# Kernel optimization log

Hardware: AMD Instinct MI355X
Metric: run time of the kernel (lower is better)

The kernel has to match this reference:

```python
import jax, jax.numpy as jnp
import numpy as np
from jax import lax

DEPTH = 5
LEAF = 2 ** DEPTH          # 32
GATES = LEAF - 1           # 31
LATENT = 128
IN_SHAPE = (128, 8, 8)     # C, H, W after mixture reshape
OUT_FEAT = IN_SHAPE[0] * IN_SHAPE[1] * IN_SHAPE[2]  # 8192
BATCH = 512


def conv_t(x, w, b):
    # PyTorch ConvTranspose2d(k=4, s=2, p=1): weight layout [in, out, kh, kw].
    # Equivalent fwd conv: flip spatial dims, swap in/out, lhs_dilation=2, pad k-1-p=2.
    w_ = jnp.flip(w, (2, 3)).transpose(1, 0, 2, 3)  # [out, in, kh, kw]
    y = lax.conv_general_dilated(
        x, w_, window_strides=(1, 1), padding=((2, 2), (2, 2)),
        lhs_dilation=(2, 2), dimension_numbers=("NCHW", "OIHW", "NCHW"))
    return y + b[None, :, None, None]


def leaf_probs_fn(x, gw, gb):
    # gatings: [B, GATES]
    g = jax.nn.sigmoid(x @ gw + gb)
    dens = jnp.ones((x.shape[0], 1), dtype=x.dtype)  # root density
    start = 0
    for d in range(1, DEPTH + 1):
        n_par = 2 ** (d - 1)
        gp = lax.dynamic_slice_in_dim(g, start, n_par, axis=1)  # [B, n_par]
        # left child (odd node index) uses g, right child uses 1-g, interleaved.
        dens = jnp.stack([dens * gp, dens * (1.0 - gp)], axis=-1).reshape(x.shape[0], 2 * n_par)
        start += n_par
    return dens  # [B, LEAF]


def setup_inputs() -> dict:
    key = jax.random.key(0)
    ks = jax.random.split(key, 10)
    C = IN_SHAPE[0]
    inp = {
        "x": jax.random.normal(ks[0], (BATCH, LATENT), dtype=jnp.float32),
        # SoftTree gating params (kaiming-normal ~ N(0, sqrt(2/fan_in)) approx)
        "gw": jax.random.normal(ks[1], (LATENT, GATES), dtype=jnp.float32) * (2.0 / LATENT) ** 0.5,
        "gb": jnp.zeros((GATES,), dtype=jnp.float32),
        # constant projection leaves
        "z": jax.random.normal(ks[2], (OUT_FEAT, LEAF), dtype=jnp.float32),
        # ConvTranspose2d weights, PyTorch layout [in_ch, out_ch, kh, kw]
        "w1": jax.random.normal(ks[3], (C, 128, 4, 4), dtype=jnp.float32) * 0.02,
        "b1": jnp.zeros((128,), dtype=jnp.float32),
        "w2": jax.random.normal(ks[4], (128, 64, 4, 4), dtype=jnp.float32) * 0.02,
        "b2": jnp.zeros((64,), dtype=jnp.float32),
        "w3": jax.random.normal(ks[5], (64, 3, 4, 4), dtype=jnp.float32) * 0.02,
        "b3": jnp.zeros((3,), dtype=jnp.float32),
    }
    return inp


def reference(x, gw, gb, z, w1, b1, w2, b2, w3, b3):
    lp = leaf_probs_fn(x, gw, gb)              # [B, LEAF]
    out = lp @ z.T                              # [B, OUT_FEAT] == (z @ lp.T).T
    out = out.reshape(-1, *IN_SHAPE)            # [B, 128, 8, 8]
    out = jax.nn.relu(conv_t(out, w1, b1))      # [B, 128, 16, 16]
    out = jax.nn.relu(conv_t(out, w2, b2))      # [B, 64, 32, 32]
    out = conv_t(out, w3, b3)                   # [B, 3, 64, 64]
    return out
```

## Files before the change

### kernel.cpp

```cpp
#include <hip/hip_runtime.h>
#include <hip/hip_bf16.h>
#include <stdint.h>

using bf16 = __hip_bfloat16;
typedef __attribute__((ext_vector_type(8))) short bf16x8;
typedef __attribute__((ext_vector_type(4))) float f32x4;
typedef __attribute__((ext_vector_type(16))) float f32x16;

#define BATCHN 512

__device__ __forceinline__ void zero_halo_dev(bf16* buf, int H, int W, int C, int idx) {
  int nvec = C >> 3;
  int P = 2 * (W + 2) + 2 * H;
  if (idx >= BATCHN * P * nvec) return;
  int cv = idx % nvec;
  int p = (idx / nvec) % P;
  int b = idx / (nvec * P);
  int row, col;
  if (p < W + 2) { row = 0; col = p; }
  else if (p < 2 * (W + 2)) { row = H + 1; col = p - (W + 2); }
  else { int q = p - 2 * (W + 2); row = 1 + (q >> 1); col = (q & 1) ? (W + 1) : 0; }
  float4 z4 = {0.f, 0.f, 0.f, 0.f};
  *(float4*)(buf + ((size_t)(b * (H + 2) + row) * (W + 2) + col) * C + cv * 8) = z4;
}

__device__ __forceinline__ void wprep_dev(const float* w, bf16* wt, int IC, int OCr, int OCp, int idx) {
  int KG = IC / 8;
  if (idx >= 16 * OCp * IC) return;
  int e = idx & 7;
  int t = idx >> 3;
  int oc = t % OCp; t /= OCp;
  int kg = t % KG; t /= KG;
  int tap = t & 3, p = t >> 2;
  int ic = kg * 8 + e;
  int dy = tap >> 1, dx = tap & 1;
  int py = p >> 1, px = p & 1;
  const int ktab[2][2] = {{1, 3}, {2, 0}};
  int ky = ktab[py][dy], kx = ktab[px][dx];
  float v = 0.f;
  if (oc < OCr) v = w[((ic * OCr + oc) * 4 + ky) * 4 + kx];
  wt[idx] = __float2bfloat16(v);
}

#define NB_Z1 1152
#define NB_Z2 2176
#define NB_Z3 2112
#define NB_W1 1024
#define NB_W2 512
#define NB_W3 64
#define NB_G  128

__global__ void prep_kernel(bf16* x1, bf16* x2, bf16* x3,
                            const float* w1, bf16* wt1, const float* w2, bf16* wt2,
                            const float* w3, bf16* wt3,
                            const float* x, const float* gw, const float* gb, float* lp) {
  int bid = blockIdx.x;
  int tid = threadIdx.x;
  if (bid < NB_Z1) { zero_halo_dev(x1, 8, 8, 128, bid * 256 + tid); return; }
  bid -= NB_Z1;
  if (bid < NB_Z2) { zero_halo_dev(x2, 16, 16, 128, bid * 256 + tid); return; }
  bid -= NB_Z2;
  if (bid < NB_Z3) { zero_halo_dev(x3, 32, 32, 64, bid * 256 + tid); return; }
  bid -= NB_Z3;
  if (bid < NB_W1) { wprep_dev(w1, wt1, 128, 128, 128, bid * 256 + tid); return; }
  bid -= NB_W1;
  if (bid < NB_W2) { wprep_dev(w2, wt2, 128, 64, 64, bid * 256 + tid); return; }
  bid -= NB_W2;
  if (bid < NB_W3) { wprep_dev(w3, wt3, 64, 3, 16, bid * 256 + tid); return; }
  bid -= NB_W3;
  __shared__ float xs[4][128];
  __shared__ float gs[4][32];
  const int sub = tid >> 6, t = tid & 63;
  const int b = bid * 4 + sub;
  xs[sub][t] = x[b * 128 + t];
  xs[sub][t + 64] = x[b * 128 + 64 + t];
  __syncthreads();
  if (t < 31) {
    float acc = gb[t];
    #pragma unroll 8
    for (int k = 0; k < 128; ++k) acc += xs[sub][k] * gw[k * 31 + t];
    gs[sub][t] = 1.f / (1.f + __expf(-acc));
  }
  __syncthreads();
  if (t < 32) {
    float prob = 1.f;
    #pragma unroll
    for (int d = 1; d <= 5; ++d) {
      int i = t >> (6 - d);
      int node = (1 << (d - 1)) - 1 + i;
      float gv = gs[sub][node];
      prob *= ((t >> (5 - d)) & 1) ? (1.f - gv) : gv;
    }
    lp[b * 32 + t] = prob;
  }
}

__global__ void mixture_kernel(const float* __restrict__ z, const float* __restrict__ lp,
                               bf16* __restrict__ x1) {
  __shared__ float lps[64 * 32];
  const int s = blockIdx.x;
  const int h = s >> 3, w = s & 7;
  const int b0 = blockIdx.y * 64;
  const int t = threadIdx.x;
  const int c = t & 127;
  const int half = t >> 7;
  float4 zr[8];
  const float4* zp = (const float4*)(z + (size_t)(c * 64 + s) * 32);
  #pragma unroll
  for (int i = 0; i < 8; ++i) zr[i] = zp[i];
  #pragma unroll
  for (int i = 0; i < 8; ++i) lps[t + 256 * i] = lp[b0 * 32 + t + 256 * i];
  __syncthreads();
  for (int bs = 0; bs < 32; ++bs) {
    int bl = half * 32 + bs;
    const float4* lr = (const float4*)(lps + bl * 32);
    float acc = 0.f;
    #pragma unroll
    for (int i = 0; i < 8; ++i) {
      float4 l4 = lr[i];
      acc += zr[i].x * l4.x + zr[i].y * l4.y + zr[i].z * l4.z + zr[i].w * l4.w;
    }
    int b = b0 + bl;
    x1[((size_t)(b * 10 + h + 1) * 10 + (w + 1)) * 128 + c] = __float2bfloat16(acc);
  }
}

#define CLASS_TABLES \
  constexpr int TAPA[9] = {0, 1, 1, 2, 2, 3, 3, 3, 3}; \
  constexpr int DYA[9]  = {0, 0, 0,-1, 1,-1,-1, 1, 1}; \
  constexpr int DXA[9]  = {0,-1, 1, 0, 0,-1, 1,-1, 1}; \
  constexpr int MSK[9]  = {0xF,0x5,0xA,0x3,0xC,0x1,0x2,0x4,0x8};

template<int IC, int OCp, int IH, int IW, int ROWS>
__global__ __launch_bounds__(256, 3)
void convt32(const bf16* __restrict__ xin, const bf16* __restrict__ wt,
             const float* __restrict__ bias, bf16* __restrict__ xout) {
  constexpr int KG = IC / 8;
  constexpr int NS = IC / 16;
  constexpr int IH2 = IH + 2, IW2 = IW + 2;
  constexpr int OH2 = 2 * IH + 2, OW2 = 2 * IW + 2;
  constexpr int NPIX = (ROWS + 2) * IW2;
  constexpr int BPI = IH / ROWS;
  constexpr int LIW = (IW == 8 ? 3 : 4);
  constexpr int ICV = IC / 8;
  __shared__ bf16 Alds[KG * NPIX * 8];

  const int tid = threadIdx.x;
  const int wave = tid >> 6, lane = tid & 63;
  const int hl = lane >> 5, l32 = lane & 31;
  const int wm = wave >> 1, wn = wave & 1;
  const int img = blockIdx.x / BPI;
  const int tb = blockIdx.x % BPI;
  const int n0 = blockIdx.y * 64;

  const bf16* src = xin + ((size_t)img * IH2 + tb * ROWS) * IW2 * IC;
  for (int g = tid; g < NPIX * ICV; g += 256) {
    const int pix = g / ICV;
    const int gr = g % ICV;
    const float4 v = *(const float4*)(src + (size_t)g * 8);
    *(float4*)(&Alds[(gr * NPIX + pix) * 8]) = v;
  }

  const int m = wm * 32 + l32;
  const int cpix = ((m >> LIW) + 1) * IW2 + (m & (IW - 1)) + 1;
  const bf16* wtp = wt + (size_t)(n0 + wn * 32 + l32) * 8;

  f32x16 acc[4];
  #pragma unroll
  for (int p = 0; p < 4; ++p)
    #pragma unroll
    for (int r = 0; r < 16; ++r) acc[p][r] = 0.f;

  CLASS_TABLES
  __syncthreads();

  #pragma unroll
  for (int e = 0; e < 9; ++e) {
    const int tap = TAPA[e];
    const int sh = (DYA[e] * IW2 + DXA[e]);
    #pragma unroll
    for (int s = 0; s < NS; ++s) {
      const bf16x8 a = *(const bf16x8*)(Alds + (((s * 2 + hl) * NPIX) + cpix + sh) * 8);
      #pragma unroll
      for (int p = 0; p < 4; ++p) {
        if (MSK[e] & (1 << p)) {
          const int chunk = p * 4 + tap;
          const bf16x8 b = *(const bf16x8*)(wtp + ((size_t)(chunk * KG + s * 2 + hl) * OCp) * 8);
          acc[p] = __builtin_amdgcn_mfma_f32_32x32x16_bf16(a, b, acc[p], 0, 0, 0);
        }
      }
    }
  }

  const int oc = n0 + wn * 32 + l32;
  const float bv = bias[oc];
  #pragma unroll
  for (int p = 0; p < 4; ++p) {
    const int py = p >> 1, px = p & 1;
    #pragma unroll
    for (int r = 0; r < 16; ++r) {
      const int ml = wm * 32 + (r & 3) + 8 * (r >> 2) + 4 * hl;
      const int y = tb * ROWS + (ml >> LIW), x = ml & (IW - 1);
      float v = fmaxf(acc[p][r] + bv, 0.f);
      xout[(((size_t)img * OH2 + 2 * y + py + 1) * OW2 + 2 * x + px + 1) * OCp + oc] =
          __float2bfloat16(v);
    }
  }
}

__global__ __launch_bounds__(256, 3)
void convt16_final(const bf16* __restrict__ xin, const bf16* __restrict__ wt,
                   const float* __restrict__ bias, float* __restrict__ fout) {
  constexpr int IC = 64, OCp = 16, OCr = 3, IH = 32, IW = 32, ROWS = 8;
  constexpr int KG = IC / 8;
  constexpr int NC = IC / 32;
  constexpr int IH2 = IH + 2, IW2 = IW + 2;
  constexpr int NPIX = (ROWS + 2) * IW2;
  constexpr int BPI = IH / ROWS;
  constexpr int MI = 4;
  constexpr int ICV = IC / 8;
  __shared__ bf16 Alds[KG * NPIX * 8];

  const int tid = threadIdx.x;
  const int wave = tid >> 6, lane = tid & 63;
  const int q = lane >> 4, li = lane & 15;
  const int img = blockIdx.x / BPI;
  const int tb = blockIdx.x % BPI;

  const bf16* src = xin + ((size_t)img * IH2 + tb * ROWS) * IW2 * IC;
  for (int g = tid; g < NPIX * ICV; g += 256) {
    const int pix = g / ICV;
    const int gr = g % ICV;
    const float4 v = *(const float4*)(src + (size_t)g * 8);
    *(float4*)(&Alds[(gr * NPIX + pix) * 8]) = v;
  }

  int cpix[MI];
  #pragma unroll
  for (int mi = 0; mi < MI; ++mi) {
    const int m = wave * 64 + mi * 16 + li;
    cpix[mi] = ((m >> 5) + 1) * IW2 + (m & 31) + 1;
  }
  const bf16* wtp = wt + (size_t)li * 8;

  f32x4 acc[4][MI];
  #pragma unroll
  for (int p = 0; p < 4; ++p)
    #pragma unroll
    for (int mi = 0; mi < MI; ++mi)
      acc[p][mi] = (f32x4){0.f, 0.f, 0.f, 0.f};

  CLASS_TABLES
  __syncthreads();

  #pragma unroll
  for (int e = 0; e < 9; ++e) {
    const int tap = TAPA[e];
    const int sh = (DYA[e] * IW2 + DXA[e]);
    #pragma unroll
    for (int c = 0; c < NC; ++c) {
      bf16x8 bfr[4];
      #pragma unroll
      for (int p = 0; p < 4; ++p)
        if (MSK[e] & (1 << p))
          bfr[p] = *(const bf16x8*)(wtp + ((size_t)((p * 4 + tap) * KG + c * 4 + q) * OCp) * 8);
      #pragma unroll
      for (int mi = 0; mi < MI; ++mi) {
        const bf16x8 a = *(const bf16x8*)(Alds + (((c * 4 + q) * NPIX) + cpix[mi] + sh) * 8);
        #pragma unroll
        for (int p = 0; p < 4; ++p)
          if (MSK[e] & (1 << p))
            acc[p][mi] = __builtin_amdgcn_mfma_f32_16x16x32_bf16(a, bfr[p], acc[p][mi], 0, 0, 0);
      }
    }
  }

  const int oc = li;
  if (oc < OCr) {
    const float bv = bias[oc];
    #pragma unroll
    for (int py = 0; py < 2; ++py)
      #pragma unroll
      for (int mi = 0; mi < MI; ++mi)
        #pragma unroll
        for (int r = 0; r < 4; ++r) {
          const int pix = (wave * MI + mi) * 16 + q * 4 + r;
          const int y = tb * ROWS + (pix >> 5), x = pix & 31;
          float2 v2;
          v2.x = acc[py * 2 + 0][mi][r] + bv;
          v2.y = acc[py * 2 + 1][mi][r] + bv;
          *(float2*)(&fout[(((size_t)img * 3 + oc) * 64 + 2 * y + py) * 64 + 2 * x]) = v2;
        }
  }
}

extern "C" void kernel_launch(void* const* d_in, const int* in_sizes, int n_in,
                              void* d_out, int out_size, void* d_ws, size_t ws_size,
                              hipStream_t stream) {
  const float* x  = (const float*)d_in[0];
  const float* gw = (const float*)d_in[1];
  const float* gb = (const float*)d_in[2];
  const float* z  = (const float*)d_in[3];
  const float* w1 = (const float*)d_in[4];
  const float* b1 = (const float*)d_in[5];
  const float* w2 = (const float*)d_in[6];
  const float* b2 = (const float*)d_in[7];
  const float* w3 = (const float*)d_in[8];
  const float* b3 = (const float*)d_in[9];
  float* out = (float*)d_out;

  char* w = (char*)d_ws;
  float* lp  = (float*)(w);
  bf16* x1  = (bf16*)(w + 65536);
  bf16* x2  = (bf16*)(w + 13172736);
  bf16* x3  = (bf16*)(w + 55640064);
  bf16* wt1 = (bf16*)(w + 131399680);
  bf16* wt2 = (bf16*)(w + 131923968);
  bf16* wt3 = (bf16*)(w + 132186112);

  prep_kernel<<<NB_Z1 + NB_Z2 + NB_Z3 + NB_W1 + NB_W2 + NB_W3 + NB_G, 256, 0, stream>>>(
      x1, x2, x3, w1, wt1, w2, wt2, w3, wt3, x, gw, gb, lp);

  mixture_kernel<<<dim3(64, 8), 256, 0, stream>>>(z, lp, x1);

  convt32<128, 128, 8, 8, 8><<<dim3(512, 2), 256, 0, stream>>>(x1, wt1, b1, x2);
  convt32<128, 64, 16, 16, 4><<<dim3(2048, 1), 256, 0, stream>>>(x2, wt2, b2, x3);
  convt16_final<<<dim3(2048, 1), 256, 0, stream>>>(x3, wt3, b3, out);
}
```

Baseline: 218.5 us.

## Restructure conv-transpose kernels so each wave owns one output parity

The first two transposed-conv layers move from a 256-thread kernel, where each wave handled a 32-row M slice across all four output parities, to a 512-thread kernel. In the new kernel each wave owns one parity and a 32-wide OC slice and accumulates several 32-row M tiles (MI). Each weight fragment is now loaded once per k-step and reused across MI MFMAs, and the next B fragment is prefetched while the current one is used. Layer 1 packs two images per block and layer 2 uses taller row tiles. The trade-off is more accumulator registers per thread (MI f32x16 accumulators) and larger LDS tiles, which may reduce occupancy.

```diff
diff --git a/kernel.cpp b/kernel.cpp
--- a/kernel.cpp
+++ b/kernel.cpp
@@ -125,84 +125,93 @@
   }
 }
 
-#define CLASS_TABLES \
-  constexpr int TAPA[9] = {0, 1, 1, 2, 2, 3, 3, 3, 3}; \
-  constexpr int DYA[9]  = {0, 0, 0,-1, 1,-1,-1, 1, 1}; \
-  constexpr int DXA[9]  = {0,-1, 1, 0, 0,-1, 1,-1, 1}; \
-  constexpr int MSK[9]  = {0xF,0x5,0xA,0x3,0xC,0x1,0x2,0x4,0x8};
-
-template<int IC, int OCp, int IH, int IW, int ROWS>
-__global__ __launch_bounds__(256, 3)
-void convt32(const bf16* __restrict__ xin, const bf16* __restrict__ wt,
-             const float* __restrict__ bias, bf16* __restrict__ xout) {
+template<int IC, int OCp, int IH, int IW, int ROWS, int IMGS>
+__global__ __launch_bounds__(512, 4)
+void convt32s(const bf16* __restrict__ xin, const bf16* __restrict__ wt,
+              const float* __restrict__ bias, bf16* __restrict__ xout) {
   constexpr int KG = IC / 8;
   constexpr int NS = IC / 16;
   constexpr int IH2 = IH + 2, IW2 = IW + 2;
   constexpr int OH2 = 2 * IH + 2, OW2 = 2 * IW + 2;
-  constexpr int NPIX = (ROWS + 2) * IW2;
+  constexpr int TPIX = (ROWS + 2) * IW2;
+  constexpr int NPIXT = IMGS * TPIX;
   constexpr int BPI = IH / ROWS;
+  constexpr int MI = IMGS * ROWS * IW / 32;
   constexpr int LIW = (IW == 8 ? 3 : 4);
   constexpr int ICV = IC / 8;
-  __shared__ bf16 Alds[KG * NPIX * 8];
+  __shared__ bf16 Alds[KG * NPIXT * 8];
 
   const int tid = threadIdx.x;
   const int wave = tid >> 6, lane = tid & 63;
-  const int hl = lane >> 5, l32 = lane & 31;
-  const int wm = wave >> 1, wn = wave & 1;
-  const int img = blockIdx.x / BPI;
-  const int tb = blockIdx.x % BPI;
-  const int n0 = blockIdx.y * 64;
-
-  const bf16* src = xin + ((size_t)img * IH2 + tb * ROWS) * IW2 * IC;
-  for (int g = tid; g < NPIX * ICV; g += 256) {
-    const int pix = g / ICV;
-    const int gr = g % ICV;
-    const float4 v = *(const float4*)(src + (size_t)g * 8);
-    *(float4*)(&Alds[(gr * NPIX + pix) * 8]) = v;
-  }
-
-  const int m = wm * 32 + l32;
-  const int cpix = ((m >> LIW) + 1) * IW2 + (m & (IW - 1)) + 1;
-  const bf16* wtp = wt + (size_t)(n0 + wn * 32 + l32) * 8;
-
-  f32x16 acc[4];
-  #pragma unroll
-  for (int p = 0; p < 4; ++p)
-    #pragma unroll
-    for (int r = 0; r < 16; ++r) acc[p][r] = 0.f;
-
-  CLASS_TABLES
-  __syncthreads();
-
-  #pragma unroll
-  for (int e = 0; e < 9; ++e) {
-    const int tap = TAPA[e];
-    const int sh = (DYA[e] * IW2 + DXA[e]);
-    #pragma unroll
-    for (int s = 0; s < NS; ++s) {
-      const bf16x8 a = *(const bf16x8*)(Alds + (((s * 2 + hl) * NPIX) + cpix + sh) * 8);
-      #pragma unroll
-      for (int p = 0; p < 4; ++p) {
-        if (MSK[e] & (1 << p)) {
-          const int chunk = p * 4 + tap;
-          const bf16x8 b = *(const bf16x8*)(wtp + ((size_t)(chunk * KG + s * 2 + hl) * OCp) * 8);
-          acc[p] = __builtin_amdgcn_mfma_f32_32x32x16_bf16(a, b, acc[p], 0, 0, 0);
-        }
-      }
-    }
-  }
-
-  const int oc = n0 + wn * 32 + l32;
+  const int l32 = lane & 31, hl = lane >> 5;
+  const int p = wave & 3, nh = wave >> 2;
+  const int py = p >> 1, px = p & 1;
+  const int bm = blockIdx.x;
+  const int img0 = (bm / BPI) * IMGS, tb = bm % BPI;
+  const int n0 = blockIdx.y * 64 + nh * 32;
+
+  #pragma unroll
+  for (int i = 0; i < IMGS; ++i) {
+    const bf16* src = xin + ((size_t)(img0 + i) * IH2 + tb * ROWS) * IW2 * IC;
+    for (int g = tid; g < TPIX * ICV; g += 512) {
+      const int pix = g / ICV;
+      const int gr = g % ICV;
+      const float4 v = *(const float4*)(src + (size_t)g * 8);
+      *(float4*)(&Alds[(gr * NPIXT + i * TPIX + pix) * 8]) = v;
+    }
+  }
+
+  const bf16* ap[MI];
+  #pragma unroll
+  for (int mi = 0; mi < MI; ++mi) {
+    const int m = mi * 32 + l32;
+    const int il = m / (ROWS * IW);
+    const int mm = m % (ROWS * IW);
+    const int pix = il * TPIX + ((mm >> LIW) + 1) * IW2 + (mm & (IW - 1)) + 1;
+    ap[mi] = Alds + ((size_t)(hl * NPIXT + pix)) * 8;
+  }
+  const bf16* wp = wt + ((size_t)((p * 4 * KG) + hl) * OCp + n0 + l32) * 8;
+
+  f32x16 acc[MI];
+  #pragma unroll
+  for (int mi = 0; mi < MI; ++mi)
+    #pragma unroll
+    for (int r = 0; r < 16; ++r) acc[mi][r] = 0.f;
+
+  auto ldB = [&](int kk) -> bf16x8 {
+    const int tap = kk >> 3, s = kk & 7;
+    return *(const bf16x8*)(wp + ((size_t)(tap * KG + s * 2) * OCp) * 8);
+  };
+
+  bf16x8 bc = ldB(0);
+  __syncthreads();
+
+  #pragma unroll
+  for (int kk = 0; kk < 4 * NS; ++kk) {
+    const bf16x8 bn = (kk + 1 < 4 * NS) ? ldB(kk + 1) : bc;
+    const int tap = kk >> 3, s = kk & 7;
+    const int dy = tap >> 1, dx = tap & 1;
+    const int sh = (dy ? (py ? 1 : -1) * IW2 : 0) + (dx ? (px ? 1 : -1) : 0);
+    #pragma unroll
+    for (int mi = 0; mi < MI; ++mi) {
+      const bf16x8 a = *(const bf16x8*)(ap[mi] + (s * 2 * NPIXT + sh) * 8);
+      acc[mi] = __builtin_amdgcn_mfma_f32_32x32x16_bf16(a, bc, acc[mi], 0, 0, 0);
+    }
+    bc = bn;
+  }
+
+  const int oc = n0 + l32;
   const float bv = bias[oc];
   #pragma unroll
-  for (int p = 0; p < 4; ++p) {
-    const int py = p >> 1, px = p & 1;
+  for (int mi = 0; mi < MI; ++mi) {
     #pragma unroll
     for (int r = 0; r < 16; ++r) {
-      const int ml = wm * 32 + (r & 3) + 8 * (r >> 2) + 4 * hl;
-      const int y = tb * ROWS + (ml >> LIW), x = ml & (IW - 1);
-      float v = fmaxf(acc[p][r] + bv, 0.f);
-      xout[(((size_t)img * OH2 + 2 * y + py + 1) * OW2 + 2 * x + px + 1) * OCp + oc] =
+      const int ml = mi * 32 + (r & 3) + 8 * (r >> 2) + 4 * hl;
+      const int il = ml / (ROWS * IW);
+      const int mm = ml % (ROWS * IW);
+      const int y = tb * ROWS + (mm >> LIW), x = mm & (IW - 1);
+      float v = fmaxf(acc[mi][r] + bv, 0.f);
+      xout[(((size_t)(img0 + il) * OH2 + 2 * y + py + 1) * OW2 + 2 * x + px + 1) * OCp + oc] =
           __float2bfloat16(v);
     }
   }
@@ -250,7 +259,10 @@
     for (int mi = 0; mi < MI; ++mi)
       acc[p][mi] = (f32x4){0.f, 0.f, 0.f, 0.f};
 
-  CLASS_TABLES
+  constexpr int TAPA[9] = {0, 1, 1, 2, 2, 3, 3, 3, 3};
+  constexpr int DYA[9]  = {0, 0, 0,-1, 1,-1,-1, 1, 1};
+  constexpr int DXA[9]  = {0,-1, 1, 0, 0,-1, 1,-1, 1};
+  constexpr int MSK[9]  = {0xF,0x5,0xA,0x3,0xC,0x1,0x2,0x4,0x8};
   __syncthreads();
 
   #pragma unroll
@@ -323,7 +335,7 @@
 
   mixture_kernel<<<dim3(64, 8), 256, 0, stream>>>(z, lp, x1);
 
-  convt32<128, 128, 8, 8, 8><<<dim3(512, 2), 256, 0, stream>>>(x1, wt1, b1, x2);
-  convt32<128, 64, 16, 16, 4><<<dim3(2048, 1), 256, 0, stream>>>(x2, wt2, b2, x3);
+  convt32s<128, 128, 8, 8, 8, 2><<<dim3(256, 2), 512, 0, stream>>>(x1, wt1, b1, x2);
+  convt32s<128, 64, 16, 16, 8, 1><<<dim3(1024, 1), 512, 0, stream>>>(x2, wt2, b2, x3);
   convt16_final<<<dim3(2048, 1), 256, 0, stream>>>(x3, wt3, b3, out);
 }
```

New measurement: 196.0 us. -10.3%, faster.

## Restructure conv-transpose kernels: per-parity waves, register B double-buffering, swizzled LDS

Applied to the files above, without the earlier changes.

The two main transposed-conv kernels now give each wave one output parity class (py,px) and a 64x64 tile (2x2 MFMAs). Previously waves were split over M and N, with every wave iterating over all nine class entries. Weight fragments are prefetched two k-steps ahead in registers, LDS addresses use an XOR swizzle to cut bank conflicts, and the launch bound rises to 4 blocks per CU. The aim is better A-fragment reuse across N, hidden global weight-load latency, and higher occupancy, at the cost of register pressure that could cause spills.

```diff
diff --git a/kernel.cpp b/kernel.cpp
--- a/kernel.cpp
+++ b/kernel.cpp
@@ -8,6 +8,8 @@
 typedef __attribute__((ext_vector_type(16))) float f32x16;
 
 #define BATCHN 512
+
+__device__ __forceinline__ int swz(int b) { return b ^ ((b >> 3) & 3); }
 
 __device__ __forceinline__ void zero_halo_dev(bf16* buf, int H, int W, int C, int idx) {
   int nvec = C >> 3;
@@ -125,18 +127,11 @@
   }
 }
 
-#define CLASS_TABLES \
-  constexpr int TAPA[9] = {0, 1, 1, 2, 2, 3, 3, 3, 3}; \
-  constexpr int DYA[9]  = {0, 0, 0,-1, 1,-1,-1, 1, 1}; \
-  constexpr int DXA[9]  = {0,-1, 1, 0, 0,-1, 1,-1, 1}; \
-  constexpr int MSK[9]  = {0xF,0x5,0xA,0x3,0xC,0x1,0x2,0x4,0x8};
-
 template<int IC, int OCp, int IH, int IW, int ROWS>
-__global__ __launch_bounds__(256, 3)
-void convt32(const bf16* __restrict__ xin, const bf16* __restrict__ wt,
-             const float* __restrict__ bias, bf16* __restrict__ xout) {
+__global__ __launch_bounds__(256, 4)
+void convt32n(const bf16* __restrict__ xin, const bf16* __restrict__ wt,
+              const float* __restrict__ bias, bf16* __restrict__ xout) {
   constexpr int KG = IC / 8;
-  constexpr int NS = IC / 16;
   constexpr int IH2 = IH + 2, IW2 = IW + 2;
   constexpr int OH2 = 2 * IH + 2, OW2 = 2 * IW + 2;
   constexpr int NPIX = (ROWS + 2) * IW2;
@@ -147,8 +142,9 @@
 
   const int tid = threadIdx.x;
   const int wave = tid >> 6, lane = tid & 63;
-  const int hl = lane >> 5, l32 = lane & 31;
-  const int wm = wave >> 1, wn = wave & 1;
+  const int l32 = lane & 31, hl = lane >> 5;
+  const int p = wave;
+  const int py = p >> 1, px = p & 1;
   const int img = blockIdx.x / BPI;
   const int tb = blockIdx.x % BPI;
   const int n0 = blockIdx.y * 64;
@@ -158,52 +154,70 @@
     const int pix = g / ICV;
     const int gr = g % ICV;
     const float4 v = *(const float4*)(src + (size_t)g * 8);
-    *(float4*)(&Alds[(gr * NPIX + pix) * 8]) = v;
-  }
-
-  const int m = wm * 32 + l32;
-  const int cpix = ((m >> LIW) + 1) * IW2 + (m & (IW - 1)) + 1;
-  const bf16* wtp = wt + (size_t)(n0 + wn * 32 + l32) * 8;
-
-  f32x16 acc[4];
-  #pragma unroll
-  for (int p = 0; p < 4; ++p)
-    #pragma unroll
-    for (int r = 0; r < 16; ++r) acc[p][r] = 0.f;
-
-  CLASS_TABLES
-  __syncthreads();
-
-  #pragma unroll
-  for (int e = 0; e < 9; ++e) {
-    const int tap = TAPA[e];
-    const int sh = (DYA[e] * IW2 + DXA[e]);
-    #pragma unroll
-    for (int s = 0; s < NS; ++s) {
-      const bf16x8 a = *(const bf16x8*)(Alds + (((s * 2 + hl) * NPIX) + cpix + sh) * 8);
-      #pragma unroll
-      for (int p = 0; p < 4; ++p) {
-        if (MSK[e] & (1 << p)) {
-          const int chunk = p * 4 + tap;
-          const bf16x8 b = *(const bf16x8*)(wtp + ((size_t)(chunk * KG + s * 2 + hl) * OCp) * 8);
-          acc[p] = __builtin_amdgcn_mfma_f32_32x32x16_bf16(a, b, acc[p], 0, 0, 0);
-        }
+    *(float4*)(&Alds[swz(gr * NPIX + pix) * 8]) = v;
+  }
+
+  int cpix[2];
+  #pragma unroll
+  for (int mi = 0; mi < 2; ++mi) {
+    const int m = mi * 32 + l32;
+    cpix[mi] = ((m >> LIW) + 1) * IW2 + (m & (IW - 1)) + 1;
+  }
+  const bf16* wp = wt + ((size_t)((p * 4 * KG) + hl) * OCp + n0 + l32) * 8;
+
+  f32x16 acc[2][2];
+  #pragma unroll
+  for (int mi = 0; mi < 2; ++mi)
+    #pragma unroll
+    for (int nj = 0; nj < 2; ++nj)
+      #pragma unroll
+      for (int r = 0; r < 16; ++r) acc[mi][nj][r] = 0.f;
+
+  auto ldB = [&](int kk, bf16x8 (&b)[2]) {
+    const int tap = kk >> 3, s = kk & 7;
+    #pragma unroll
+    for (int nj = 0; nj < 2; ++nj)
+      b[nj] = *(const bf16x8*)(wp + ((size_t)((tap * KG + s * 2) * OCp) + nj * 32) * 8);
+  };
+
+  bf16x8 bb[2][2];
+  ldB(0, bb[0]);
+  ldB(1, bb[1]);
+  __syncthreads();
+
+  const int sh_y = (py ? 1 : -1) * IW2;
+  const int sh_x = (px ? 1 : -1);
+
+  #pragma unroll
+  for (int kk = 0; kk < 32; ++kk) {
+    const int tap = kk >> 3, s = kk & 7;
+    const int sh = ((tap >> 1) ? sh_y : 0) + ((tap & 1) ? sh_x : 0);
+    bf16x8 a[2];
+    #pragma unroll
+    for (int mi = 0; mi < 2; ++mi)
+      a[mi] = *(const bf16x8*)(&Alds[swz((s * 2 + hl) * NPIX + cpix[mi] + sh) * 8]);
+    #pragma unroll
+    for (int mi = 0; mi < 2; ++mi)
+      #pragma unroll
+      for (int nj = 0; nj < 2; ++nj)
+        acc[mi][nj] = __builtin_amdgcn_mfma_f32_32x32x16_bf16(a[mi], bb[kk & 1][nj], acc[mi][nj], 0, 0, 0);
+    if (kk + 2 < 32) ldB(kk + 2, bb[kk & 1]);
+  }
+
+  #pragma unroll
+  for (int nj = 0; nj < 2; ++nj) {
+    const int oc = n0 + nj * 32 + l32;
+    const float bv = bias[oc];
+    #pragma unroll
+    for (int mi = 0; mi < 2; ++mi) {
+      #pragma unroll
+      for (int r = 0; r < 16; ++r) {
+        const int ml = mi * 32 + (r & 3) + 8 * (r >> 2) + 4 * hl;
+        const int y = tb * ROWS + (ml >> LIW), x = ml & (IW - 1);
+        float v = fmaxf(acc[mi][nj][r] + bv, 0.f);
+        xout[(((size_t)img * OH2 + 2 * y + py + 1) * OW2 + 2 * x + px + 1) * OCp + oc] =
+            __float2bfloat16(v);
       }
-    }
-  }
-
-  const int oc = n0 + wn * 32 + l32;
-  const float bv = bias[oc];
-  #pragma unroll
-  for (int p = 0; p < 4; ++p) {
-    const int py = p >> 1, px = p & 1;
-    #pragma unroll
-    for (int r = 0; r < 16; ++r) {
-      const int ml = wm * 32 + (r & 3) + 8 * (r >> 2) + 4 * hl;
-      const int y = tb * ROWS + (ml >> LIW), x = ml & (IW - 1);
-      float v = fmaxf(acc[p][r] + bv, 0.f);
-      xout[(((size_t)img * OH2 + 2 * y + py + 1) * OW2 + 2 * x + px + 1) * OCp + oc] =
-          __float2bfloat16(v);
     }
   }
 }
@@ -250,7 +264,10 @@
     for (int mi = 0; mi < MI; ++mi)
       acc[p][mi] = (f32x4){0.f, 0.f, 0.f, 0.f};
 
-  CLASS_TABLES
+  constexpr int TAPA[9] = {0, 1, 1, 2, 2, 3, 3, 3, 3};
+  constexpr int DYA[9]  = {0, 0, 0,-1, 1,-1,-1, 1, 1};
+  constexpr int DXA[9]  = {0,-1, 1, 0, 0,-1, 1,-1, 1};
+  constexpr int MSK[9]  = {0xF,0x5,0xA,0x3,0xC,0x1,0x2,0x4,0x8};
   __syncthreads();
 
   #pragma unroll
@@ -323,7 +340,7 @@
 
   mixture_kernel<<<dim3(64, 8), 256, 0, stream>>>(z, lp, x1);
 
-  convt32<128, 128, 8, 8, 8><<<dim3(512, 2), 256, 0, stream>>>(x1, wt1, b1, x2);
-  convt32<128, 64, 16, 16, 4><<<dim3(2048, 1), 256, 0, stream>>>(x2, wt2, b2, x3);
+  convt32n<128, 128, 8, 8, 8><<<dim3(512, 2), 256, 0, stream>>>(x1, wt1, b1, x2);
+  convt32n<128, 64, 16, 16, 4><<<dim3(2048, 1), 256, 0, stream>>>(x2, wt2, b2, x3);
   convt16_final<<<dim3(2048, 1), 256, 0, stream>>>(x3, wt3, b3, out);
 }
```

Result: no change. 217.3 us (-0.5%).
